# Performance work log

Measured on AMD Instinct MI355X. Metric: run time of the kernel, lower is better.

Reference implementation:

```python
import jax, jax.numpy as jnp
import numpy as np

B, CIN, COUT, H, W = 8, 128, 256, 64, 64
EPS = 1e-5


def conv2d(x, w, b, pad):
    y = jax.lax.conv_general_dilated(
        x, w, window_strides=(1, 1), padding=[(pad, pad), (pad, pad)],
        dimension_numbers=('NCHW', 'OIHW', 'NCHW'))
    return y + b[None, :, None, None]


def deform_sample(x, offset):
    # x: [B,C,H,W], offset: [B,18,H,W] -> sampled: [B,C,9,H,W]
    b, c, h, w = x.shape
    off = offset.reshape(b, 9, 2, h, w)  # (dy, dx) per kernel tap (torchvision v1 order)
    ky = (jnp.arange(9) // 3 - 1).astype(x.dtype)
    kx = (jnp.arange(9) % 3 - 1).astype(x.dtype)
    py = jnp.arange(h, dtype=x.dtype)[None, None, :, None] + ky[None, :, None, None] + off[:, :, 0]
    px = jnp.arange(w, dtype=x.dtype)[None, None, None, :] + kx[None, :, None, None] + off[:, :, 1]
    y0 = jnp.floor(py); x0 = jnp.floor(px)
    fy = py - y0;       fx = px - x0
    xf = x.reshape(b, c, h * w)

    def gather(iy, ix):
        valid = (iy >= 0) & (iy < h) & (ix >= 0) & (ix < w)
        iyc = jnp.clip(iy, 0, h - 1).astype(jnp.int32)
        ixc = jnp.clip(ix, 0, w - 1).astype(jnp.int32)
        idx = (iyc * w + ixc).reshape(b, -1)  # [B, 9*H*W]
        g = jax.vmap(lambda xb, ib: jnp.take(xb, ib, axis=1))(xf, idx)  # [B,C,9HW]
        return g.reshape(b, c, 9, h, w) * valid.astype(x.dtype)[:, None]

    samp = (gather(y0,     x0    ) * ((1 - fy) * (1 - fx))[:, None]
          + gather(y0,     x0 + 1) * ((1 - fy) * fx      )[:, None]
          + gather(y0 + 1, x0    ) * (fy * (1 - fx)      )[:, None]
          + gather(y0 + 1, x0 + 1) * (fy * fx            )[:, None])
    return samp


def setup_inputs():
    key = jax.random.key(0)
    ks = jax.random.split(key, 8)
    return {
        'x':     jax.random.normal(ks[0], (B, CIN, H, W), jnp.float32),
        'w_off': jax.random.normal(ks[1], (18, CIN, 3, 3), jnp.float32) * 0.01,
        'b_off': jnp.zeros((18,), jnp.float32),
        'w_def': jax.random.normal(ks[2], (COUT, CIN, 3, 3), jnp.float32) * 0.03,
        'b_def': jax.random.normal(ks[3], (COUT,), jnp.float32) * 0.01,
        'gamma': jnp.ones((COUT,), jnp.float32),
        'beta':  jnp.zeros((COUT,), jnp.float32),
        'w_sc':  jax.random.normal(ks[4], (COUT, CIN, 1, 1), jnp.float32) * 0.05,
        'b_sc':  jnp.zeros((COUT,), jnp.float32),
    }


def reference(x, w_off, b_off, w_def, b_def, gamma, beta, w_sc, b_sc):
    offset = conv2d(x, w_off, b_off, pad=1)                 # [B,18,H,W]
    samp = deform_sample(x, offset)                         # [B,C,9,H,W]
    out = jnp.einsum('bckhw,ock->bohw', samp, w_def.reshape(COUT, CIN, 9))
    out = out + b_def[None, :, None, None]
    # BatchNorm2d (training mode: batch statistics)
    mean = out.mean(axis=(0, 2, 3))
    var = out.var(axis=(0, 2, 3))
    out = (out - mean[None, :, None, None]) * jax.lax.rsqrt(var + EPS)[None, :, None, None]
    out = out * gamma[None, :, None, None] + beta[None, :, None, None]
    out = out + conv2d(x, w_sc, b_sc, pad=0)                # residual shortcut (1x1)
    return jax.nn.relu(out)
```

## Files before the change

### kernel.cpp

```cpp
#include <hip/hip_runtime.h>

typedef __attribute__((ext_vector_type(8))) short bf16x8;
typedef __attribute__((ext_vector_type(4))) float f32x4;

__device__ __forceinline__ float bf2f(unsigned short u) {
  return __uint_as_float(((unsigned int)u) << 16);
}
__device__ __forceinline__ unsigned short f2bf(float f) {
  unsigned int u = __float_as_uint(f);
  u += 0x7fffu + ((u >> 16) & 1u);
  return (unsigned short)(u >> 16);
}

constexpr size_t OFF_XPAD = 0;
constexpr size_t SZ_XPAD  = (size_t)8 * 66 * 66 * 128 * 2;
constexpr size_t OFF_WB   = OFF_XPAD + SZ_XPAD;
constexpr size_t SZ_WB    = (size_t)9 * 16 * 256 * 8 * 2;
constexpr size_t OFF_WS2  = OFF_WB + SZ_WB;
constexpr size_t SZ_WS2   = (size_t)16 * 256 * 8 * 2;
constexpr size_t OFF_WO   = OFF_WS2 + SZ_WS2;
constexpr size_t SZ_WO    = (size_t)9 * 16 * 32 * 8 * 2;
constexpr size_t OFF_YM   = OFF_WO + SZ_WO;
constexpr size_t SZ_YM    = (size_t)32768 * 256 * 2;
constexpr size_t OFF_SR   = OFF_YM + SZ_YM;
constexpr size_t SZ_SR    = (size_t)8 * 256 * 2 * 4;


__global__ __launch_bounds__(256) void k_prep(const float* __restrict__ x,
                                              unsigned short* __restrict__ xp,
                                              const float* __restrict__ wdef,
                                              const float* __restrict__ wsc,
                                              const float* __restrict__ woff,
                                              unsigned short* __restrict__ wB,
                                              unsigned short* __restrict__ wS,
                                              unsigned short* __restrict__ wO,
                                              float* __restrict__ statsRaw) {
  int t = threadIdx.x;
  if (blockIdx.x == 1936) {
    for (int i = t; i < 4096; i += 256) statsRaw[i] = 0.f;
    return;
  }
  if (blockIdx.x >= 512) {
    int tid = (blockIdx.x - 512) * 256 + t;
    if (tid < 294912) {
      int k8 = tid & 7, n = (tid >> 3) & 255, kb = (tid >> 11) & 15, tap = tid >> 15;
      int c = kb * 8 + k8;
      wB[tid] = f2bf(wdef[((size_t)n * 128 + c) * 9 + tap]);
    } else if (tid < 294912 + 32768) {
      int i = tid - 294912;
      int k8 = i & 7, n = (i >> 3) & 255, kb = i >> 11;
      wS[i] = f2bf(wsc[(size_t)n * 128 + kb * 8 + k8]);
    } else if (tid < 294912 + 32768 + 36864) {
      int i = tid - 327680;
      int k8 = i & 7, n = (i >> 3) & 31, kb = (i >> 8) & 15, tap = i >> 12;
      int c = kb * 8 + k8;
      wO[i] = f2bf(n < 18 ? woff[((size_t)n * 128 + c) * 9 + tap] : 0.f);
    }
    return;
  }
  int blk = blockIdx.x;
  int b = blk & 7, h = blk >> 3;
  __shared__ unsigned short xt[128 * 68];
  {
    unsigned short* base = xp + (size_t)b * 66 * 66 * 128;
    ushort4 z4 = {0, 0, 0, 0};
    if (t < 64) {
      int col = (t >> 5) ? 65 : 0;
      int i = t & 31;
      *(ushort4*)(base + ((size_t)(h + 1) * 66 + col) * 128 + i * 4) = z4;
    }
    if (h == 0) {
      for (int i = t; i < 2112; i += 256) {
        *(ushort4*)(base + (size_t)i * 4) = z4;
        *(ushort4*)(base + (size_t)65 * 66 * 128 + (size_t)i * 4) = z4;
      }
    }
  }
  {
    int c = t >> 1, w0 = (t & 1) * 32;
    const float4* xs = (const float4*)&x[(((size_t)b * 128 + c) * 64 + h) * 64 + w0];
    unsigned short* row = &xt[c * 68 + w0];
#pragma unroll
    for (int i4 = 0; i4 < 8; ++i4) {
      float4 f = xs[i4];
      ushort4 u4;
      u4.x = f2bf(f.x); u4.y = f2bf(f.y); u4.z = f2bf(f.z); u4.w = f2bf(f.w);
      *(ushort4*)(row + i4 * 4) = u4;
    }
  }
  __syncthreads();
  {
    int w = t >> 2, c0 = (t & 3) * 32;
    unsigned short tmp[32];
#pragma unroll
    for (int i = 0; i < 32; ++i) tmp[i] = xt[(c0 + i) * 68 + w];
    unsigned short* dst = xp + ((size_t)(b * 66 + h + 1) * 66 + (w + 1)) * 128 + c0;
#pragma unroll
    for (int i8 = 0; i8 < 4; ++i8)
      *(bf16x8*)(dst + i8 * 8) = *(const bf16x8*)&tmp[i8 * 8];
  }
}

__global__ __launch_bounds__(512, 4) void k_main(const unsigned short* __restrict__ xp,
                                                 const unsigned short* __restrict__ wB,
                                                 const unsigned short* __restrict__ wO,
                                                 const float* __restrict__ boff,
                                                 const float* __restrict__ bdef,
                                                 unsigned short* __restrict__ ymain,
                                                 float* __restrict__ statsRaw) {
  int blk = blockIdx.x;
  int b = blk & 7, h = blk >> 3;
  int bh = (b << 6) + h;
  int t = threadIdx.x;
  int lane = t & 63, wid = t >> 6;
  int m = lane & 15, quad = lane >> 4;
  __shared__ __align__(16) unsigned short At[2][64 * 136];
  __shared__ float offsL[9][64][2];

  if (wid < 4) {
    f32x4 a0 = {0.f, 0.f, 0.f, 0.f}, a1 = {0.f, 0.f, 0.f, 0.f};
    int px = wid * 16 + m;
    const unsigned short* xbase = xp + ((size_t)(b * 66 + h) * 66 + px) * 128 + quad * 8;
    for (int tap = 0; tap < 9; ++tap) {
      const unsigned short* arow = xbase + ((tap / 3) * 66 + (tap % 3)) * 128;
#pragma unroll
      for (int kk = 0; kk < 4; ++kk) {
        bf16x8 a = *(const bf16x8*)(arow + kk * 32);
        const unsigned short* bb = wO + (size_t)(tap * 16 + kk * 4 + quad) * 256;
        bf16x8 b0 = *(const bf16x8*)(bb + m * 8);
        bf16x8 b1 = *(const bf16x8*)(bb + (16 + m) * 8);
        a0 = __builtin_amdgcn_mfma_f32_16x16x32_bf16(a, b0, a0, 0, 0, 0);
        a1 = __builtin_amdgcn_mfma_f32_16x16x32_bf16(a, b1, a1, 0, 0, 0);
      }
    }
#pragma unroll
    for (int r = 0; r < 4; ++r) {
      int pxs = wid * 16 + quad * 4 + r;
      offsL[m >> 1][pxs][m & 1] = a0[r] + boff[m];
      if (m < 2) offsL[8][pxs][m] = a1[r] + boff[16 + m];
    }
  }

  f32x4 acc[4][2];
#pragma unroll
  for (int i = 0; i < 4; ++i)
#pragma unroll
    for (int j = 0; j < 2; ++j) acc[i][j] = (f32x4){0.f, 0.f, 0.f, 0.f};

  int px_s = t >> 3, sub = t & 7;
  const unsigned short* xb_base = xp + (size_t)b * 66 * 66 * 128;
  int nb = wid * 32;

  bf16x8 Breg[4][2];
  auto loadB = [&](int tap) {
#pragma unroll
    for (int kk = 0; kk < 4; ++kk)
#pragma unroll
      for (int ns = 0; ns < 2; ++ns)
        Breg[kk][ns] = *(const bf16x8*)(wB + ((size_t)(tap * 16 + kk * 4 + quad) * 256 + nb + ns * 16 + m) * 8);
  };

  auto sample_prep = [&](int tap, float* wgt, const unsigned short** p) {
    float2 ov = *(const float2*)&offsL[tap][px_s][0];
    int ky = tap / 3 - 1, kx = tap % 3 - 1;
    float py = (float)(h + ky) + ov.x;
    float pxf = (float)(px_s + kx) + ov.y;
    float y0f = floorf(py), x0f = floorf(pxf);
    float fy = py - y0f, fx = pxf - x0f;
    int iy0 = (int)y0f, ix0 = (int)x0f;
#pragma unroll
    for (int j = 0; j < 4; ++j) {
      int iy = iy0 + (j >> 1), ix = ix0 + (j & 1);
      float wy = (j >> 1) ? fy : 1.f - fy;
      float wx = (j & 1) ? fx : 1.f - fx;
      bool valid = (iy >= 0) && (iy < 64) && (ix >= 0) && (ix < 64);
      int iyc = min(max(iy, 0), 63), ixc = min(max(ix, 0), 63);
      wgt[j] = valid ? wy * wx : 0.f;
      p[j] = xb_base + ((size_t)(iyc + 1) * 66 + (ixc + 1)) * 128 + sub * 8;
    }
  };
  auto load_g1 = [&](const unsigned short** p, int g, bf16x8* v) {
#pragma unroll
    for (int j = 0; j < 4; ++j)
      v[j] = *(const bf16x8*)(p[j] + g * 64);
  };
  auto store_g1 = [&](unsigned short* dst, int g, const float* wgt, bf16x8* v) {
    bf16x8 o;
#pragma unroll
    for (int j = 0; j < 8; ++j) {
      float s = fmaf(wgt[0], bf2f((unsigned short)v[0][j]),
                fmaf(wgt[1], bf2f((unsigned short)v[1][j]),
                fmaf(wgt[2], bf2f((unsigned short)v[2][j]),
                     wgt[3] * bf2f((unsigned short)v[3][j]))));
      o[j] = (short)f2bf(s);
    }
    *(bf16x8*)(dst + g * 64) = o;
  };
  auto mfma_half = [&](const unsigned short* buf, int kk0) {
#pragma unroll
    for (int kk = kk0; kk < kk0 + 2; ++kk) {
      bf16x8 af[4];
#pragma unroll
      for (int ms = 0; ms < 4; ++ms)
        af[ms] = *(const bf16x8*)(buf + (ms * 16 + m) * 136 + kk * 32 + quad * 8);
#pragma unroll
      for (int ns = 0; ns < 2; ++ns)
#pragma unroll
        for (int ms = 0; ms < 4; ++ms)
          acc[ms][ns] = __builtin_amdgcn_mfma_f32_16x16x32_bf16(af[ms], Breg[kk][ns], acc[ms][ns], 0, 0, 0);
    }
  };

  loadB(0);
  __syncthreads();
  {
    float wgt[4]; const unsigned short* p[4]; bf16x8 v0[4], v1[4];
    sample_prep(0, wgt, p);
    unsigned short* dst = &At[0][px_s * 136 + sub * 8];
    load_g1(p, 0, v0); load_g1(p, 1, v1);
    store_g1(dst, 0, wgt, v0); store_g1(dst, 1, wgt, v1);
  }
#pragma unroll
  for (int tap = 0; tap < 9; ++tap) {
    __syncthreads();
    const unsigned short* cur = At[tap & 1];
    unsigned short* dst = &At[(tap + 1) & 1][px_s * 136 + sub * 8];
    if (tap < 8) {
      float wgt[4]; const unsigned short* p[4]; bf16x8 v0[4], v1[4];
      sample_prep(tap + 1, wgt, p);
      load_g1(p, 0, v0);
      load_g1(p, 1, v1);
      mfma_half(cur, 0);
      store_g1(dst, 0, wgt, v0);
      mfma_half(cur, 2);
      loadB(tap + 1);
      store_g1(dst, 1, wgt, v1);
    } else {
      mfma_half(cur, 0);
      mfma_half(cur, 2);
    }
  }

  __syncthreads();
  unsigned short* yb = &At[0][0];
#pragma unroll
  for (int ns = 0; ns < 2; ++ns) {
    int n = nb + ns * 16 + m;
    float bias = bdef[n];
    float s = 0.f, q = 0.f;
#pragma unroll
    for (int ms = 0; ms < 4; ++ms) {
#pragma unroll
      for (int r = 0; r < 4; ++r) {
        int px = ms * 16 + quad * 4 + r;
        float v = acc[ms][ns][r] + bias;
        yb[px * 264 + n] = f2bf(v);
        s += v;
        q += v * v;
      }
    }
    s += __shfl_xor(s, 16); s += __shfl_xor(s, 32);
    q += __shfl_xor(q, 16); q += __shfl_xor(q, 32);
    if (quad == 0) {
      atomicAdd(&statsRaw[((size_t)b * 256 + n) * 2 + 0], s);
      atomicAdd(&statsRaw[((size_t)b * 256 + n) * 2 + 1], q);
    }
  }
  __syncthreads();
  {
    unsigned short* grow = ymain + (size_t)(bh * 64 + px_s) * 256;
    const unsigned short* lrow = yb + px_s * 264;
#pragma unroll
    for (int k = 0; k < 4; ++k) {
      int n0 = k * 64 + sub * 8;
      __builtin_nontemporal_store(*(const bf16x8*)(lrow + n0), (bf16x8*)(grow + n0));
    }
  }
}

__global__ __launch_bounds__(256) void k_final(const unsigned short* __restrict__ xp,
                                               const unsigned short* __restrict__ wS,
                                               const unsigned short* __restrict__ ymain,
                                               const float* __restrict__ statsRaw,
                                               const float* __restrict__ gamma,
                                               const float* __restrict__ beta,
                                               const float* __restrict__ bsc,
                                               float* __restrict__ out) {
  int blk = blockIdx.x;
  int b = blk & 7, rem = blk >> 3, h = rem >> 1, half = rem & 1;
  int px0 = half * 32;
  int bh = (b << 6) + h;
  int t = threadIdx.x;
  int lane = t & 63, wid = t >> 6;
  int m = lane & 15, quad = lane >> 4;
  __shared__ float tr[128 * 35];
  __shared__ float sAB[512];
  {
    float s = 0.f, q = 0.f;
#pragma unroll
    for (int i = 0; i < 8; ++i) {
      float2 pq = *(const float2*)&statsRaw[((size_t)i * 256 + t) * 2];
      s += pq.x;
      q += pq.y;
    }
    float mean = s * (1.f / 32768.f);
    float var = q * (1.f / 32768.f) - mean * mean;
    float inv = rsqrtf(var + 1e-5f);
    float A = gamma[t] * inv;
    sAB[t] = A;
    sAB[256 + t] = beta[t] - mean * A;
  }
  f32x4 acc[2][4];
#pragma unroll
  for (int i = 0; i < 2; ++i)
#pragma unroll
    for (int j = 0; j < 4; ++j) acc[i][j] = (f32x4){0.f, 0.f, 0.f, 0.f};
  const unsigned short* xrow = xp + ((size_t)(b * 66 + h + 1) * 66 + 1 + px0) * 128;
  int nb = wid * 64;
#pragma unroll
  for (int kk = 0; kk < 4; ++kk) {
    bf16x8 af[2];
#pragma unroll
    for (int ms = 0; ms < 2; ++ms)
      af[ms] = *(const bf16x8*)(xrow + (ms * 16 + m) * 128 + kk * 32 + quad * 8);
#pragma unroll
    for (int ns = 0; ns < 4; ++ns) {
      bf16x8 bfr = *(const bf16x8*)(wS + ((size_t)(kk * 4 + quad) * 256 + nb + ns * 16 + m) * 8);
#pragma unroll
      for (int ms = 0; ms < 2; ++ms)
        acc[ms][ns] = __builtin_amdgcn_mfma_f32_16x16x32_bf16(af[ms], bfr, acc[ms][ns], 0, 0, 0);
    }
  }
  __syncthreads();
  for (int pass = 0; pass < 2; ++pass) {
    if ((wid >> 1) == pass) {
#pragma unroll
      for (int ns = 0; ns < 4; ++ns) {
        int n = nb + ns * 16 + m;
        float bs = bsc[n];
        int nl = n - pass * 128;
#pragma unroll
        for (int ms = 0; ms < 2; ++ms)
#pragma unroll
          for (int r = 0; r < 4; ++r) {
            int px = ms * 16 + quad * 4 + r;
            tr[nl * 35 + px] = acc[ms][ns][r] + bs;
          }
      }
    }
    __syncthreads();
    {
      int nl2 = t & 63, g = t >> 6;
      int n = pass * 128 + nl2 * 2;
      float A0 = sAB[n], B0 = sAB[256 + n];
      float A1 = sAB[n + 1], B1 = sAB[256 + n + 1];
#pragma unroll
      for (int i = 0; i < 8; ++i) {
        int pxl = g * 8 + i;
        unsigned int ym2 = *(const unsigned int*)(ymain + (size_t)(bh * 64 + px0 + pxl) * 256 + n);
        float y0 = bf2f((unsigned short)(ym2 & 0xffffu));
        float y1 = bf2f((unsigned short)(ym2 >> 16));
        int nl = nl2 * 2;
        float* p0 = &tr[nl * 35 + pxl];
        float* p1 = &tr[(nl + 1) * 35 + pxl];
        *p0 = fmaxf(fmaf(y0, A0, B0) + *p0, 0.f);
        *p1 = fmaxf(fmaf(y1, A1, B1) + *p1, 0.f);
      }
    }
    __syncthreads();
    {
      int ww = t & 31, ng = t >> 5;
#pragma unroll
      for (int i = 0; i < 16; ++i) {
        int nl = ng * 16 + i;
        out[((size_t)(b * 256 + pass * 128 + nl) * 64 + h) * 64 + px0 + ww] = tr[nl * 35 + ww];
      }
    }
    __syncthreads();
  }
}

extern "C" void kernel_launch(void* const* d_in, const int* in_sizes, int n_in,
                              void* d_out, int out_size, void* d_ws, size_t ws_size,
                              hipStream_t stream) {
  const float* x     = (const float*)d_in[0];
  const float* w_off = (const float*)d_in[1];
  const float* b_off = (const float*)d_in[2];
  const float* w_def = (const float*)d_in[3];
  const float* b_def = (const float*)d_in[4];
  const float* gamma = (const float*)d_in[5];
  const float* beta  = (const float*)d_in[6];
  const float* w_sc  = (const float*)d_in[7];
  const float* b_sc  = (const float*)d_in[8];
  float* out = (float*)d_out;

  char* ws = (char*)d_ws;
  unsigned short* xpad  = (unsigned short*)(ws + OFF_XPAD);
  unsigned short* wB    = (unsigned short*)(ws + OFF_WB);
  unsigned short* wS    = (unsigned short*)(ws + OFF_WS2);
  unsigned short* wO    = (unsigned short*)(ws + OFF_WO);
  unsigned short* ymain = (unsigned short*)(ws + OFF_YM);
  float* statsRaw       = (float*)(ws + OFF_SR);

  k_prep<<<1937, 256, 0, stream>>>(x, xpad, w_def, w_sc, w_off, wB, wS, wO, statsRaw);
  k_main<<<512, 512, 0, stream>>>(xpad, wB, wO, b_off, b_def, ymain, statsRaw);
  k_final<<<1024, 256, 0, stream>>>(xpad, wS, ymain, statsRaw, gamma, beta, b_sc, out);
}
```

Baseline: 149.5 us.

## Store main output in MFMA fragment layout and restructure final epilogue

The main kernel now writes its pre-BN activations directly from MFMA accumulator registers in a per-thread fragment order, dropping the LDS transpose and two barriers. The final kernel is relaunched with 512-thread blocks covering a full row, reads those fragments contiguously, fuses BN, shortcut and ReLU in registers, then writes coalesced vector stores through LDS. Weight prep packs 8 bf16 per thread with vector stores, and the x transpose uses coalesced float4 reads. This couples the two kernels' thread mappings and adds register pressure in the final kernel.

```diff
diff --git a/kernel.cpp b/kernel.cpp
--- a/kernel.cpp
+++ b/kernel.cpp
@@ -21,7 +21,7 @@
 constexpr size_t OFF_WO   = OFF_WS2 + SZ_WS2;
 constexpr size_t SZ_WO    = (size_t)9 * 16 * 32 * 8 * 2;
 constexpr size_t OFF_YM   = OFF_WO + SZ_WO;
-constexpr size_t SZ_YM    = (size_t)32768 * 256 * 2;
+constexpr size_t SZ_YM    = (size_t)512 * 512 * 32 * 2;
 constexpr size_t OFF_SR   = OFF_YM + SZ_YM;
 constexpr size_t SZ_SR    = (size_t)8 * 256 * 2 * 4;
 
@@ -36,25 +36,33 @@
                                               unsigned short* __restrict__ wO,
                                               float* __restrict__ statsRaw) {
   int t = threadIdx.x;
-  if (blockIdx.x == 1936) {
+  if (blockIdx.x == 690) {
     for (int i = t; i < 4096; i += 256) statsRaw[i] = 0.f;
     return;
   }
   if (blockIdx.x >= 512) {
-    int tid = (blockIdx.x - 512) * 256 + t;
-    if (tid < 294912) {
-      int k8 = tid & 7, n = (tid >> 3) & 255, kb = (tid >> 11) & 15, tap = tid >> 15;
-      int c = kb * 8 + k8;
-      wB[tid] = f2bf(wdef[((size_t)n * 128 + c) * 9 + tap]);
-    } else if (tid < 294912 + 32768) {
-      int i = tid - 294912;
-      int k8 = i & 7, n = (i >> 3) & 255, kb = i >> 11;
-      wS[i] = f2bf(wsc[(size_t)n * 128 + kb * 8 + k8]);
-    } else if (tid < 294912 + 32768 + 36864) {
-      int i = tid - 327680;
-      int k8 = i & 7, n = (i >> 3) & 31, kb = (i >> 8) & 15, tap = i >> 12;
-      int c = kb * 8 + k8;
-      wO[i] = f2bf(n < 18 ? woff[((size_t)n * 128 + c) * 9 + tap] : 0.f);
+    int base = ((blockIdx.x - 512) * 256 + t) * 8;
+    unsigned short w8[8];
+    if (base < 294912) {
+      int n = (base >> 3) & 255, kb = (base >> 11) & 15, tap = base >> 15;
+#pragma unroll
+      for (int j = 0; j < 8; ++j)
+        w8[j] = f2bf(wdef[((size_t)n * 128 + kb * 8 + j) * 9 + tap]);
+      *(bf16x8*)(wB + base) = *(const bf16x8*)w8;
+    } else if (base < 327680) {
+      int i0 = base - 294912;
+      int n = (i0 >> 3) & 255, kb = i0 >> 11;
+#pragma unroll
+      for (int j = 0; j < 8; ++j)
+        w8[j] = f2bf(wsc[(size_t)n * 128 + kb * 8 + j]);
+      *(bf16x8*)(wS + i0) = *(const bf16x8*)w8;
+    } else {
+      int i0 = base - 327680;
+      int n = (i0 >> 3) & 31, kb = (i0 >> 8) & 15, tap = i0 >> 12;
+#pragma unroll
+      for (int j = 0; j < 8; ++j)
+        w8[j] = f2bf(n < 18 ? woff[((size_t)n * 128 + kb * 8 + j) * 9 + tap] : 0.f);
+      *(bf16x8*)(wO + i0) = *(const bf16x8*)w8;
     }
     return;
   }
@@ -77,24 +85,23 @@
     }
   }
   {
-    int c = t >> 1, w0 = (t & 1) * 32;
-    const float4* xs = (const float4*)&x[(((size_t)b * 128 + c) * 64 + h) * 64 + w0];
-    unsigned short* row = &xt[c * 68 + w0];
 #pragma unroll
     for (int i4 = 0; i4 < 8; ++i4) {
-      float4 f = xs[i4];
+      int idx = t + i4 * 256;
+      int row = idx >> 4, col = (idx & 15) * 4;
+      float4 f = *(const float4*)&x[(((size_t)b * 128 + row) * 64 + h) * 64 + col];
       ushort4 u4;
       u4.x = f2bf(f.x); u4.y = f2bf(f.y); u4.z = f2bf(f.z); u4.w = f2bf(f.w);
-      *(ushort4*)(row + i4 * 4) = u4;
+      *(ushort4*)&xt[row * 68 + col] = u4;
     }
   }
   __syncthreads();
   {
-    int w = t >> 2, c0 = (t & 3) * 32;
+    int w = t & 63, cg = t >> 6;
     unsigned short tmp[32];
 #pragma unroll
-    for (int i = 0; i < 32; ++i) tmp[i] = xt[(c0 + i) * 68 + w];
-    unsigned short* dst = xp + ((size_t)(b * 66 + h + 1) * 66 + (w + 1)) * 128 + c0;
+    for (int i = 0; i < 32; ++i) tmp[i] = xt[(cg * 32 + i) * 68 + w];
+    unsigned short* dst = xp + ((size_t)(b * 66 + h + 1) * 66 + (w + 1)) * 128 + cg * 32;
 #pragma unroll
     for (int i8 = 0; i8 < 4; ++i8)
       *(bf16x8*)(dst + i8 * 8) = *(const bf16x8*)&tmp[i8 * 8];
@@ -110,7 +117,6 @@
                                                  float* __restrict__ statsRaw) {
   int blk = blockIdx.x;
   int b = blk & 7, h = blk >> 3;
-  int bh = (b << 6) + h;
   int t = threadIdx.x;
   int lane = t & 63, wid = t >> 6;
   int m = lane & 15, quad = lane >> 4;
@@ -241,24 +247,20 @@
     }
   }
 
-  __syncthreads();
-  unsigned short* yb = &At[0][0];
 #pragma unroll
   for (int ns = 0; ns < 2; ++ns) {
     int n = nb + ns * 16 + m;
     float bias = bdef[n];
     float s = 0.f, q = 0.f;
 #pragma unroll
-    for (int ms = 0; ms < 4; ++ms) {
+    for (int ms = 0; ms < 4; ++ms)
 #pragma unroll
       for (int r = 0; r < 4; ++r) {
-        int px = ms * 16 + quad * 4 + r;
         float v = acc[ms][ns][r] + bias;
-        yb[px * 264 + n] = f2bf(v);
+        acc[ms][ns][r] = v;
         s += v;
         q += v * v;
       }
-    }
     s += __shfl_xor(s, 16); s += __shfl_xor(s, 32);
     q += __shfl_xor(q, 16); q += __shfl_xor(q, 32);
     if (quad == 0) {
@@ -266,36 +268,38 @@
       atomicAdd(&statsRaw[((size_t)b * 256 + n) * 2 + 1], q);
     }
   }
-  __syncthreads();
-  {
-    unsigned short* grow = ymain + (size_t)(bh * 64 + px_s) * 256;
-    const unsigned short* lrow = yb + px_s * 264;
-#pragma unroll
-    for (int k = 0; k < 4; ++k) {
-      int n0 = k * 64 + sub * 8;
-      __builtin_nontemporal_store(*(const bf16x8*)(lrow + n0), (bf16x8*)(grow + n0));
-    }
-  }
-}
-
-__global__ __launch_bounds__(256) void k_final(const unsigned short* __restrict__ xp,
-                                               const unsigned short* __restrict__ wS,
-                                               const unsigned short* __restrict__ ymain,
-                                               const float* __restrict__ statsRaw,
-                                               const float* __restrict__ gamma,
-                                               const float* __restrict__ beta,
-                                               const float* __restrict__ bsc,
-                                               float* __restrict__ out) {
+  {
+    unsigned short yfrag[32];
+#pragma unroll
+    for (int ns = 0; ns < 2; ++ns)
+#pragma unroll
+      for (int ms = 0; ms < 4; ++ms)
+#pragma unroll
+        for (int r = 0; r < 4; ++r)
+          yfrag[ns * 16 + ms * 4 + r] = f2bf(acc[ms][ns][r]);
+    unsigned short* dst = ymain + ((size_t)blk * 512 + t) * 32;
+#pragma unroll
+    for (int k = 0; k < 4; ++k)
+      __builtin_nontemporal_store(*(const bf16x8*)&yfrag[k * 8], (bf16x8*)(dst + k * 8));
+  }
+}
+
+__global__ __launch_bounds__(512, 4) void k_final(const unsigned short* __restrict__ xp,
+                                                  const unsigned short* __restrict__ wS,
+                                                  const unsigned short* __restrict__ ymain,
+                                                  const float* __restrict__ statsRaw,
+                                                  const float* __restrict__ gamma,
+                                                  const float* __restrict__ beta,
+                                                  const float* __restrict__ bsc,
+                                                  float* __restrict__ out) {
   int blk = blockIdx.x;
-  int b = blk & 7, rem = blk >> 3, h = rem >> 1, half = rem & 1;
-  int px0 = half * 32;
-  int bh = (b << 6) + h;
+  int b = blk & 7, h = blk >> 3;
   int t = threadIdx.x;
   int lane = t & 63, wid = t >> 6;
   int m = lane & 15, quad = lane >> 4;
-  __shared__ float tr[128 * 35];
+  __shared__ __align__(16) float tr[128 * 68];
   __shared__ float sAB[512];
-  {
+  if (t < 256) {
     float s = 0.f, q = 0.f;
 #pragma unroll
     for (int i = 0; i < 8; ++i) {
@@ -310,70 +314,63 @@
     sAB[t] = A;
     sAB[256 + t] = beta[t] - mean * A;
   }
-  f32x4 acc[2][4];
-#pragma unroll
-  for (int i = 0; i < 2; ++i)
-#pragma unroll
-    for (int j = 0; j < 4; ++j) acc[i][j] = (f32x4){0.f, 0.f, 0.f, 0.f};
-  const unsigned short* xrow = xp + ((size_t)(b * 66 + h + 1) * 66 + 1 + px0) * 128;
-  int nb = wid * 64;
+  f32x4 accS[4][2];
+#pragma unroll
+  for (int i = 0; i < 4; ++i)
+#pragma unroll
+    for (int j = 0; j < 2; ++j) accS[i][j] = (f32x4){0.f, 0.f, 0.f, 0.f};
+  const unsigned short* xrow = xp + ((size_t)(b * 66 + h + 1) * 66 + 1) * 128;
+  int nb = wid * 32;
 #pragma unroll
   for (int kk = 0; kk < 4; ++kk) {
-    bf16x8 af[2];
-#pragma unroll
-    for (int ms = 0; ms < 2; ++ms)
+    bf16x8 af[4];
+#pragma unroll
+    for (int ms = 0; ms < 4; ++ms)
       af[ms] = *(const bf16x8*)(xrow + (ms * 16 + m) * 128 + kk * 32 + quad * 8);
 #pragma unroll
-    for (int ns = 0; ns < 4; ++ns) {
+    for (int ns = 0; ns < 2; ++ns) {
       bf16x8 bfr = *(const bf16x8*)(wS + ((size_t)(kk * 4 + quad) * 256 + nb + ns * 16 + m) * 8);
 #pragma unroll
-      for (int ms = 0; ms < 2; ++ms)
-        acc[ms][ns] = __builtin_amdgcn_mfma_f32_16x16x32_bf16(af[ms], bfr, acc[ms][ns], 0, 0, 0);
-    }
+      for (int ms = 0; ms < 4; ++ms)
+        accS[ms][ns] = __builtin_amdgcn_mfma_f32_16x16x32_bf16(af[ms], bfr, accS[ms][ns], 0, 0, 0);
+    }
+  }
+  bf16x8 yf[4];
+  {
+    const unsigned short* ysrc = ymain + ((size_t)blk * 512 + t) * 32;
+#pragma unroll
+    for (int k = 0; k < 4; ++k)
+      yf[k] = __builtin_nontemporal_load((const bf16x8*)(ysrc + k * 8));
   }
   __syncthreads();
+  int pass_own = wid >> 2;
   for (int pass = 0; pass < 2; ++pass) {
-    if ((wid >> 1) == pass) {
-#pragma unroll
-      for (int ns = 0; ns < 4; ++ns) {
+    if (pass_own == pass) {
+#pragma unroll
+      for (int ns = 0; ns < 2; ++ns) {
         int n = nb + ns * 16 + m;
-        float bs = bsc[n];
+        float A = sAB[n], Bc = sAB[256 + n], bs = bsc[n];
         int nl = n - pass * 128;
 #pragma unroll
-        for (int ms = 0; ms < 2; ++ms)
+        for (int ms = 0; ms < 4; ++ms)
 #pragma unroll
           for (int r = 0; r < 4; ++r) {
-            int px = ms * 16 + quad * 4 + r;
-            tr[nl * 35 + px] = acc[ms][ns][r] + bs;
+            int e = ns * 16 + ms * 4 + r;
+            float y = bf2f((unsigned short)yf[e >> 3][e & 7]);
+            float v = fmaf(y, A, Bc) + accS[ms][ns][r] + bs;
+            tr[nl * 68 + ms * 16 + quad * 4 + r] = fmaxf(v, 0.f);
           }
       }
     }
     __syncthreads();
     {
-      int nl2 = t & 63, g = t >> 6;
-      int n = pass * 128 + nl2 * 2;
-      float A0 = sAB[n], B0 = sAB[256 + n];
-      float A1 = sAB[n + 1], B1 = sAB[256 + n + 1];
-#pragma unroll
-      for (int i = 0; i < 8; ++i) {
-        int pxl = g * 8 + i;
-        unsigned int ym2 = *(const unsigned int*)(ymain + (size_t)(bh * 64 + px0 + pxl) * 256 + n);
-        float y0 = bf2f((unsigned short)(ym2 & 0xffffu));
-        float y1 = bf2f((unsigned short)(ym2 >> 16));
-        int nl = nl2 * 2;
-        float* p0 = &tr[nl * 35 + pxl];
-        float* p1 = &tr[(nl + 1) * 35 + pxl];
-        *p0 = fmaxf(fmaf(y0, A0, B0) + *p0, 0.f);
-        *p1 = fmaxf(fmaf(y1, A1, B1) + *p1, 0.f);
-      }
-    }
-    __syncthreads();
-    {
-      int ww = t & 31, ng = t >> 5;
-#pragma unroll
-      for (int i = 0; i < 16; ++i) {
-        int nl = ng * 16 + i;
-        out[((size_t)(b * 256 + pass * 128 + nl) * 64 + h) * 64 + px0 + ww] = tr[nl * 35 + ww];
+      int nl = t >> 2, q4 = t & 3;
+      float* orow = out + ((size_t)(b * 256 + pass * 128 + nl) * 64 + h) * 64 + q4 * 16;
+      const float* lrow = &tr[nl * 68 + q4 * 16];
+#pragma unroll
+      for (int i4 = 0; i4 < 4; ++i4) {
+        f32x4 v = *(const f32x4*)(lrow + i4 * 4);
+        __builtin_nontemporal_store(v, (f32x4*)(orow + i4 * 4));
       }
     }
     __syncthreads();
@@ -402,7 +399,7 @@
   unsigned short* ymain = (unsigned short*)(ws + OFF_YM);
   float* statsRaw       = (float*)(ws + OFF_SR);
 
-  k_prep<<<1937, 256, 0, stream>>>(x, xpad, w_def, w_sc, w_off, wB, wS, wO, statsRaw);
+  k_prep<<<691, 256, 0, stream>>>(x, xpad, w_def, w_sc, w_off, wB, wS, wO, statsRaw);
   k_main<<<512, 512, 0, stream>>>(xpad, wB, wO, b_off, b_def, ymain, statsRaw);
-  k_final<<<1024, 256, 0, stream>>>(xpad, wS, ymain, statsRaw, gamma, beta, b_sc, out);
-}
+  k_final<<<512, 512, 0, stream>>>(xpad, wS, ymain, statsRaw, gamma, beta, b_sc, out);
+}
```

Result: slower. 219.5 us (+46.8%).
